# Optimization experiments

Hardware: AMD Instinct MI355X
Metric: run time of the kernel (lower is better)

The kernel has to match this reference:

```python
import jax, jax.numpy as jnp
import numpy as np

N_NODES = 50000
N_EDGES = 600000
IN_F = 128
HID = 128
OUT = 128
CLS = 128
N_GRAPHS = 64
LN_EPS = 1e-5


def _ln(h, g, b):
    m = jnp.mean(h, axis=-1, keepdims=True)
    v = jnp.var(h, axis=-1, keepdims=True)
    return (h - m) * jax.lax.rsqrt(v + LN_EPS) * g + b


def _segment_softmax(logits, seg, num_segments):
    m = jax.ops.segment_max(logits, seg, num_segments=num_segments)
    e = jnp.exp(logits - m[seg])
    s = jax.ops.segment_sum(e, seg, num_segments=num_segments)
    return e / s[seg]


def _gat_conv(x, src, dst, aux, w_lin, b_lin, aw1, ab1, lng, lnb, aw2, ab2):
    xl = x @ w_lin + b_lin                      # [N, out]
    sf = xl[src]                                # [E, out]
    df = xl[dst]                                # [E, out]
    ef = jnp.concatenate([sf, df, aux], axis=-1)  # [E, 2*out+2]
    h = jax.nn.relu(_ln(ef @ aw1 + ab1, lng, lnb))
    logits = h @ aw2 + ab2                      # [E, 1]
    att = _segment_softmax(logits, dst, xl.shape[0])
    num = jax.ops.segment_sum(sf * att, dst, num_segments=xl.shape[0])
    cnt = jax.ops.segment_sum(jnp.ones((src.shape[0], 1), xl.dtype), dst, num_segments=xl.shape[0])
    out = num / jnp.maximum(cnt, 1.0)           # scatter_mean (empty rows -> 0)
    return out + xl


def setup_inputs() -> dict:
    key = jax.random.key(0)
    ks = jax.random.split(key, 24)
    s = 0.05
    d = {
        'x': jax.random.normal(ks[0], (N_NODES, IN_F), jnp.float32),
        'edge_index': jax.random.randint(ks[1], (2, N_EDGES), 0, N_NODES, jnp.int64),
        'aux_info': jax.random.normal(ks[2], (N_EDGES, 2), jnp.float32),
        'batch': jnp.sort(jax.random.randint(ks[3], (N_NODES,), 0, N_GRAPHS, jnp.int64)),
        # conv1 params (in->hid)
        'w_lin1': jax.random.normal(ks[4], (IN_F, HID), jnp.float32) * s,
        'b_lin1': jnp.zeros((HID,), jnp.float32),
        'aw1_1': jax.random.normal(ks[5], (2 * HID + 2, HID), jnp.float32) * s,
        'ab1_1': jnp.zeros((HID,), jnp.float32),
        'lng1': jnp.ones((HID,), jnp.float32),
        'lnb1': jnp.zeros((HID,), jnp.float32),
        'aw2_1': jax.random.normal(ks[6], (HID, 1), jnp.float32) * s,
        'ab2_1': jnp.zeros((1,), jnp.float32),
        # conv2 params (hid->out)
        'w_lin2': jax.random.normal(ks[7], (HID, OUT), jnp.float32) * s,
        'b_lin2': jnp.zeros((OUT,), jnp.float32),
        'aw1_2': jax.random.normal(ks[8], (2 * OUT + 2, HID), jnp.float32) * s,
        'ab1_2': jnp.zeros((HID,), jnp.float32),
        'lng2': jnp.ones((HID,), jnp.float32),
        'lnb2': jnp.zeros((HID,), jnp.float32),
        'aw2_2': jax.random.normal(ks[9], (HID, 1), jnp.float32) * s,
        'ab2_2': jnp.zeros((1,), jnp.float32),
        # head
        'cls_w': jax.random.normal(ks[10], (OUT, CLS), jnp.float32) * s,
        'cls_b': jnp.zeros((CLS,), jnp.float32),
        'norm_g': jnp.ones((OUT,), jnp.float32),
        'norm_b': jnp.zeros((OUT,), jnp.float32),
    }
    return d


def reference(x, edge_index, aux_info, batch,
              w_lin1, b_lin1, aw1_1, ab1_1, lng1, lnb1, aw2_1, ab2_1,
              w_lin2, b_lin2, aw1_2, ab1_2, lng2, lnb2, aw2_2, ab2_2,
              cls_w, cls_b, norm_g, norm_b):
    src, dst = edge_index[0], edge_index[1]
    h = _gat_conv(x, src, dst, aux_info, w_lin1, b_lin1, aw1_1, ab1_1, lng1, lnb1, aw2_1, ab2_1)
    h = jax.nn.relu(h)
    h = _gat_conv(h, src, dst, aux_info, w_lin2, b_lin2, aw1_2, ab1_2, lng2, lnb2, aw2_2, ab2_2)
    h = _ln(h, norm_g, norm_b)                  # [N, out]
    fusion = jax.ops.segment_max(h, batch, num_segments=N_GRAPHS)  # global max pool
    cls = fusion @ cls_w + cls_b                # [G, cls]
    return (h, cls)
```

## Files before the change

kernel.cpp:

```cpp
#include <hip/hip_runtime.h>
#include <math.h>

typedef __attribute__((ext_vector_type(8))) short short8v;
typedef __attribute__((ext_vector_type(4))) float f32x4;
typedef __attribute__((ext_vector_type(2))) float f32x2;

__device__ __forceinline__ unsigned short f2bf(float f) {
    union { float f; unsigned int u; } v; v.f = f;
    unsigned int r = v.u + 0x7FFFu + ((v.u >> 16) & 1u);
    return (unsigned short)(r >> 16);
}
__device__ __forceinline__ float bflo(unsigned int v) {
    union { unsigned int u; float f; } x; x.u = v << 16; return x.f;
}
__device__ __forceinline__ float bfhi(unsigned int v) {
    union { unsigned int u; float f; } x; x.u = v & 0xFFFF0000u; return x.f;
}
__device__ __forceinline__ unsigned char f2fp8(float f) {
    return (unsigned char)(__builtin_amdgcn_cvt_pk_fp8_f32(f, f, 0, false) & 0xFF);
}

__global__ void hist_kernel(const int* __restrict__ dst, int* __restrict__ deg, int E) {
    int e = blockIdx.x * 256 + threadIdx.x;
    if (e < E) atomicAdd(&deg[dst[e]], 1);
}

__global__ __launch_bounds__(256) void scan1_kernel(const int* __restrict__ deg,
                                                    int* __restrict__ rp,
                                                    int* __restrict__ bsum, int N) {
    const int lane = threadIdx.x & 63, wid = threadIdx.x >> 6;
    int i = blockIdx.x * 256 + threadIdx.x;
    int v = (i < N) ? deg[i] : 0;
    int val = v;
#pragma unroll
    for (int off = 1; off < 64; off <<= 1) {
        int t = __shfl_up(val, off, 64);
        if (lane >= off) val += t;
    }
    __shared__ int ws[4];
    if (lane == 63) ws[wid] = val;
    __syncthreads();
    int pre = 0;
#pragma unroll
    for (int w = 0; w < 4; ++w) pre += (w < wid) ? ws[w] : 0;
    int incl = pre + val;
    if (i < N) rp[i] = incl - v;
    if (threadIdx.x == 255) bsum[blockIdx.x] = incl;
}

__global__ __launch_bounds__(256) void scan2_kernel(int* __restrict__ bsum, int NB) {
    const int lane = threadIdx.x & 63, wid = threadIdx.x >> 6;
    int t = threadIdx.x;
    int v = (t < NB) ? bsum[t] : 0;
    int val = v;
#pragma unroll
    for (int off = 1; off < 64; off <<= 1) {
        int t2 = __shfl_up(val, off, 64);
        if (lane >= off) val += t2;
    }
    __shared__ int ws[4];
    if (lane == 63) ws[wid] = val;
    __syncthreads();
    int pre = 0;
#pragma unroll
    for (int w = 0; w < 4; ++w) pre += (w < wid) ? ws[w] : 0;
    int excl = pre + val - v;
    __syncthreads();
    if (t < NB) bsum[t] = excl;
}

__global__ __launch_bounds__(256) void scan3_kernel(int* __restrict__ rp,
                                                    const int* __restrict__ bsum,
                                                    int N, int E) {
    int i = blockIdx.x * 256 + threadIdx.x;
    if (i < N) rp[i] += bsum[blockIdx.x];
    if (i == 0) rp[N] = E;
}

__global__ void scatter_kernel(const int* __restrict__ src, const int* __restrict__ dst,
                               const float* __restrict__ aux,
                               const int* __restrict__ rowptr, int* __restrict__ cursor,
                               uint2* __restrict__ er, int E) {
    int e = blockIdx.x * 256 + threadIdx.x;
    if (e < E) {
        int d = dst[e];
        int pos = rowptr[d] + atomicAdd(&cursor[d], 1);
        float2 a = *(const float2*)(aux + 2 * e);
        uint2 r;
        r.x = (unsigned)src[e] | ((unsigned)d << 16);
        r.y = (unsigned)f2bf(a.x) | ((unsigned)f2bf(a.y) << 16);
        er[pos] = r;
    }
}

__global__ void bounds_kernel(const int* __restrict__ batch, int* __restrict__ gstart,
                              int* __restrict__ gend, int N) {
    int i = blockIdx.x * 256 + threadIdx.x;
    if (i >= N) return;
    int b = batch[i];
    if (i == 0 || batch[i - 1] != b) gstart[b] = i;
    if (i == N - 1 || batch[i + 1] != b) gend[b] = i + 1;
}

__global__ __launch_bounds__(256) void pack6_kernel(const float* __restrict__ s0,
                                                    const float* __restrict__ s1,
                                                    const float* __restrict__ s2,
                                                    const float* __restrict__ s3,
                                                    const float* __restrict__ s4,
                                                    const float* __restrict__ s5,
                                                    unsigned short* __restrict__ Wp) {
    int which = blockIdx.x >> 6;
    const float* W = (which == 0) ? s0 : (which == 1) ? s1 : (which == 2) ? s2
                   : (which == 3) ? s3 : (which == 4) ? s4 : s5;
    int t = (blockIdx.x & 63) * 256 + threadIdx.x;
    int j = t & 7, l = (t >> 3) & 63, ct = (t >> 9) & 7, ks = t >> 12;
    int k = ks * 32 + (l >> 4) * 8 + j;
    int n = ct * 16 + (l & 15);
    Wp[which * 16384 + t] = f2bf(W[k * 128 + n]);
}

template <int ABF>
__global__ __launch_bounds__(256) void linpq_kernel(const void* __restrict__ Av,
                                                    const unsigned short* __restrict__ WpL,
                                                    const float* __restrict__ bias,
                                                    const unsigned short* __restrict__ WpP,
                                                    const unsigned short* __restrict__ WpQ,
                                                    const float* __restrict__ ab1,
                                                    unsigned short* __restrict__ Dbf,
                                                    unsigned char* __restrict__ Vf8,
                                                    unsigned char* __restrict__ Pf8,
                                                    unsigned char* __restrict__ Qf8, int M) {
    __shared__ unsigned short lds[32][136];
    const int l = threadIdx.x & 63, w = threadIdx.x >> 6;
    const int tile = w >> 1, ch = w & 1;
    const int rowbase = blockIdx.x * 32 + tile * 16;
    const int r = rowbase + (l & 15);
    const int kc = (l >> 4) * 8;

    short8v afr[4];
    if (r < M) {
        if (ABF) {
            const unsigned short* ap = (const unsigned short*)Av + (size_t)r * 128 + kc;
#pragma unroll
            for (int ks = 0; ks < 4; ++ks)
                afr[ks] = *(const short8v*)(ap + ks * 32);
        } else {
            const float* ap = (const float*)Av + (size_t)r * 128 + kc;
#pragma unroll
            for (int ks = 0; ks < 4; ++ks) {
                float4 x0 = *(const float4*)(ap + ks * 32);
                float4 x1 = *(const float4*)(ap + ks * 32 + 4);
                unsigned short u[8] = {f2bf(x0.x), f2bf(x0.y), f2bf(x0.z), f2bf(x0.w),
                                       f2bf(x1.x), f2bf(x1.y), f2bf(x1.z), f2bf(x1.w)};
                afr[ks] = *(short8v*)u;
            }
        }
    } else {
#pragma unroll
        for (int ks = 0; ks < 4; ++ks)
#pragma unroll
            for (int j = 0; j < 8; ++j) afr[ks][j] = 0;
    }

    f32x4 acc[4];
#pragma unroll
    for (int c = 0; c < 4; ++c)
#pragma unroll
        for (int j = 0; j < 4; ++j) acc[c][j] = 0.f;

    const short8v* wl = (const short8v*)WpL;
#pragma unroll
    for (int ks = 0; ks < 4; ++ks)
#pragma unroll
        for (int c = 0; c < 4; ++c)
            acc[c] = __builtin_amdgcn_mfma_f32_16x16x32_bf16(
                afr[ks], wl[(ks * 8 + ch * 4 + c) * 64 + l], acc[c], 0, 0, 0);

    const int rb = rowbase + (l >> 4) * 4;
    const int lrb = tile * 16 + (l >> 4) * 4;
#pragma unroll
    for (int c = 0; c < 4; ++c) {
        int col = (ch * 4 + c) * 16 + (l & 15);
        float bv = bias ? bias[col] : 0.f;
#pragma unroll
        for (int j = 0; j < 4; ++j) {
            int row = rb + j;
            if (row < M) {
                float v = acc[c][j] + bv;
                unsigned short bf = f2bf(v);
                Dbf[(size_t)row * 128 + col] = bf;
                Vf8[(size_t)row * 128 + col] = f2fp8(v);
                lds[lrb + j][col] = bf;
            } else {
                lds[lrb + j][col] = 0;
            }
        }
    }
    __syncthreads();

    short8v xfr[4];
#pragma unroll
    for (int ks = 0; ks < 4; ++ks)
        xfr[ks] = *(const short8v*)&lds[tile * 16 + (l & 15)][kc + ks * 32];

    f32x4 accP[4], accQ[4];
#pragma unroll
    for (int c = 0; c < 4; ++c)
#pragma unroll
        for (int j = 0; j < 4; ++j) { accP[c][j] = 0.f; accQ[c][j] = 0.f; }

    const short8v* wp = (const short8v*)WpP;
    const short8v* wq = (const short8v*)WpQ;
#pragma unroll
    for (int ks = 0; ks < 4; ++ks)
#pragma unroll
        for (int c = 0; c < 4; ++c) {
            accP[c] = __builtin_amdgcn_mfma_f32_16x16x32_bf16(
                xfr[ks], wp[(ks * 8 + ch * 4 + c) * 64 + l], accP[c], 0, 0, 0);
            accQ[c] = __builtin_amdgcn_mfma_f32_16x16x32_bf16(
                xfr[ks], wq[(ks * 8 + ch * 4 + c) * 64 + l], accQ[c], 0, 0, 0);
        }

#pragma unroll
    for (int c = 0; c < 4; ++c) {
        int col = (ch * 4 + c) * 16 + (l & 15);
        float b1v = ab1[col];
#pragma unroll
        for (int j = 0; j < 4; ++j) {
            int row = rb + j;
            if (row < M) {
                Pf8[(size_t)row * 128 + col] = f2fp8(accP[c][j]);
                Qf8[(size_t)row * 128 + col] = f2fp8(accQ[c][j] + b1v);
            }
        }
    }
}

__global__ __launch_bounds__(256, 4) void attn_edge_kernel(
    const unsigned char* __restrict__ Pf8, const unsigned char* __restrict__ Qf8,
    const uint2* __restrict__ er,
    const float* __restrict__ wa0, const float* __restrict__ wa1,
    const float* __restrict__ lng, const float* __restrict__ lnb,
    const float* __restrict__ aw2, const float* __restrict__ ab2,
    float* __restrict__ wt, int E) {
    __shared__ float lwp[640];
    for (int idx = threadIdx.x; idx < 640; idx += 256) {
        int arr = idx >> 7;
        int rem = idx & 127;
        int par = rem >> 6;
        int c = (rem >> 2) & 15;
        int e = rem & 3;
        const float* sp = (arr == 0) ? wa0 : (arr == 1) ? wa1 : (arr == 2) ? lng
                        : (arr == 3) ? lnb : aw2;
        lwp[(((arr * 16 + c) << 1) + par) * 4 + e] = sp[rem];
    }
    __syncthreads();
    const int slot = blockIdx.x * 128 + ((int)threadIdx.x >> 1);
    if (slot >= E) return;
    const int par = threadIdx.x & 1;
    const int co = par << 6;

#define LWP(arr, c) (*(const float4*)&lwp[((((arr) * 16 + (c)) << 1) + par) * 4])

    uint2 ev = er[slot];
    const int sn = (int)(ev.x & 0xFFFFu);
    const int dn = (int)(ev.x >> 16);
    const float ax = bflo(ev.y), ay = bfhi(ev.y);

    const uint4* prow = (const uint4*)(Pf8 + (size_t)sn * 128 + co);
    const uint4* qrow = (const uint4*)(Qf8 + (size_t)dn * 128 + co);

    float r1 = 0.f, r2 = 0.f;
    unsigned tp[32];

#pragma unroll
    for (int g = 0; g < 4; ++g) {
        uint4 pv = prow[g];
        uint4 qv = qrow[g];
        unsigned pwa[4] = {pv.x, pv.y, pv.z, pv.w};
        unsigned qwa[4] = {qv.x, qv.y, qv.z, qv.w};
#pragma unroll
        for (int cc = 0; cc < 4; ++cc) {
            const int c = g * 4 + cc;
            f32x2 plo = __builtin_amdgcn_cvt_pk_f32_fp8((int)pwa[cc], false);
            f32x2 phi = __builtin_amdgcn_cvt_pk_f32_fp8((int)pwa[cc], true);
            f32x2 qlo = __builtin_amdgcn_cvt_pk_f32_fp8((int)qwa[cc], false);
            f32x2 qhi = __builtin_amdgcn_cvt_pk_f32_fp8((int)qwa[cc], true);
            float4 w0v = LWP(0, c);
            float4 w1v = LWP(1, c);
            float t0 = plo[0] + qlo[0] + ax * w0v.x + ay * w1v.x;
            float t1 = plo[1] + qlo[1] + ax * w0v.y + ay * w1v.y;
            float t2 = phi[0] + qhi[0] + ax * w0v.z + ay * w1v.z;
            float t3 = phi[1] + qhi[1] + ax * w0v.w + ay * w1v.w;
            r1 += (t0 + t1) + (t2 + t3);
            r2 = fmaf(t0, t0, r2); r2 = fmaf(t1, t1, r2);
            r2 = fmaf(t2, t2, r2); r2 = fmaf(t3, t3, r2);
            asm("v_cvt_pk_bf16_f32 %0, %1, %2" : "=v"(tp[2 * c]) : "v"(t0), "v"(t1));
            asm("v_cvt_pk_bf16_f32 %0, %1, %2" : "=v"(tp[2 * c + 1]) : "v"(t2), "v"(t3));
        }
    }
    r1 += __shfl_xor(r1, 1, 64);
    r2 += __shfl_xor(r2, 1, 64);
    float mean = r1 * (1.f / 128.f);
    float rstd = rsqrtf(r2 * (1.f / 128.f) - mean * mean + 1e-5f);
    float mr = mean * rstd;

    float dot = 0.f;
#pragma unroll
    for (int c = 0; c < 16; ++c) {
        float4 gv = LWP(2, c);
        float4 bv = LWP(3, c);
        float4 wv = LWP(4, c);
        float t0 = bflo(tp[2 * c]), t1 = bfhi(tp[2 * c]);
        float t2 = bflo(tp[2 * c + 1]), t3 = bfhi(tp[2 * c + 1]);
        float h0 = fmaxf(fmaf(fmaf(t0, rstd, -mr), gv.x, bv.x), 0.f);
        float h1 = fmaxf(fmaf(fmaf(t1, rstd, -mr), gv.y, bv.y), 0.f);
        float h2 = fmaxf(fmaf(fmaf(t2, rstd, -mr), gv.z, bv.z), 0.f);
        float h3 = fmaxf(fmaf(fmaf(t3, rstd, -mr), gv.w, bv.w), 0.f);
        dot = fmaf(h0, wv.x, dot); dot = fmaf(h1, wv.y, dot);
        dot = fmaf(h2, wv.z, dot); dot = fmaf(h3, wv.w, dot);
    }
#undef LWP
    dot += __shfl_xor(dot, 1, 64);
    if (par == 0) wt[slot] = __expf(dot + ab2[0]);
}

template <int MODE>
__global__ __launch_bounds__(256) void aggr_kernel(
    const unsigned short* __restrict__ xlbf, const unsigned char* __restrict__ Vf8,
    const float* __restrict__ wt,
    const uint2* __restrict__ er, const int* __restrict__ rowptr,
    const float* __restrict__ g, const float* __restrict__ b,
    void* __restrict__ out, int N) {
    const int lane8 = threadIdx.x & 7;
    const int v = blockIdx.x * 32 + ((int)threadIdx.x >> 3);
    if (v >= N) return;
    const int jb = lane8 * 16;

    const int s0 = rowptr[v], s1e = rowptr[v + 1];
    const int deg = s1e - s0;
    float acc[16];
#pragma unroll
    for (int k = 0; k < 16; ++k) acc[k] = 0.f;
    float wsum = 0.f;

    uint4 v0 = make_uint4(0, 0, 0, 0), v1 = v0;
    float wb0 = 0.f, wb1 = 0.f;
#define GATH2(idx, VV, WW)                                                       \
    if ((idx) < s1e) {                                                           \
        int sn_ = (int)(er[idx].x & 0xFFFFu);                                    \
        VV = *(const uint4*)(Vf8 + (size_t)sn_ * 128 + jb);                      \
        WW = wt[idx];                                                            \
    }
    GATH2(s0, v0, wb0)
    GATH2(s0 + 1, v1, wb1)

    for (int i = s0; i < s1e; i += 2) {
        uint4 c0 = v0, c1 = v1;
        float u0 = wb0;
        float u1 = (i + 1 < s1e) ? wb1 : 0.f;
        GATH2(i + 2, v0, wb0)
        GATH2(i + 3, v1, wb1)
        wsum += u0 + u1;
        unsigned d0[4] = {c0.x, c0.y, c0.z, c0.w};
        unsigned d1[4] = {c1.x, c1.y, c1.z, c1.w};
#pragma unroll
        for (int k = 0; k < 4; ++k) {
            f32x2 alo = __builtin_amdgcn_cvt_pk_f32_fp8((int)d0[k], false);
            f32x2 ahi = __builtin_amdgcn_cvt_pk_f32_fp8((int)d0[k], true);
            f32x2 blo = __builtin_amdgcn_cvt_pk_f32_fp8((int)d1[k], false);
            f32x2 bhi = __builtin_amdgcn_cvt_pk_f32_fp8((int)d1[k], true);
            acc[4 * k + 0] += u0 * alo[0] + u1 * blo[0];
            acc[4 * k + 1] += u0 * alo[1] + u1 * blo[1];
            acc[4 * k + 2] += u0 * ahi[0] + u1 * bhi[0];
            acc[4 * k + 3] += u0 * ahi[1] + u1 * bhi[1];
        }
    }
#undef GATH2

    const float ns = (deg > 0) ? 1.f / (wsum * (float)deg) : 0.f;
    float o[16];
    const unsigned short* xp = xlbf + (size_t)v * 128 + jb;
    uint4 xa = *(const uint4*)xp;
    uint4 xb = *(const uint4*)(xp + 8);
    unsigned xw[8] = {xa.x, xa.y, xa.z, xa.w, xb.x, xb.y, xb.z, xb.w};
#pragma unroll
    for (int k = 0; k < 8; ++k) {
        o[2 * k] = bflo(xw[k]) + acc[2 * k] * ns;
        o[2 * k + 1] = bfhi(xw[k]) + acc[2 * k + 1] * ns;
    }

    if (MODE == 0) {
        unsigned short* op = (unsigned short*)out + (size_t)v * 128 + jb;
        unsigned opk[8];
#pragma unroll
        for (int k = 0; k < 8; ++k)
            opk[k] = (unsigned)f2bf(fmaxf(o[2 * k], 0.f)) |
                     ((unsigned)f2bf(fmaxf(o[2 * k + 1], 0.f)) << 16);
        *(uint4*)op = make_uint4(opk[0], opk[1], opk[2], opk[3]);
        *(uint4*)(op + 8) = make_uint4(opk[4], opk[5], opk[6], opk[7]);
    } else {
        float r1 = 0.f, r2 = 0.f;
#pragma unroll
        for (int k = 0; k < 16; ++k) { r1 += o[k]; r2 = fmaf(o[k], o[k], r2); }
#pragma unroll
        for (int mk = 4; mk >= 1; mk >>= 1) {
            r1 += __shfl_xor(r1, mk, 64);
            r2 += __shfl_xor(r2, mk, 64);
        }
        float mean = r1 * (1.f / 128.f);
        float rstd = rsqrtf(r2 * (1.f / 128.f) - mean * mean + 1e-5f);
        float mr = mean * rstd;
        float* op = (float*)out + (size_t)v * 128 + jb;
#pragma unroll
        for (int k4 = 0; k4 < 4; ++k4) {
            float4 gv = *(const float4*)(g + jb + 4 * k4);
            float4 bv = *(const float4*)(b + jb + 4 * k4);
            float4 r;
            r.x = fmaf(fmaf(o[4 * k4 + 0], rstd, -mr), gv.x, bv.x);
            r.y = fmaf(fmaf(o[4 * k4 + 1], rstd, -mr), gv.y, bv.y);
            r.z = fmaf(fmaf(o[4 * k4 + 2], rstd, -mr), gv.z, bv.z);
            r.w = fmaf(fmaf(o[4 * k4 + 3], rstd, -mr), gv.w, bv.w);
            *(float4*)(op + 4 * k4) = r;
        }
    }
}

__global__ __launch_bounds__(128) void pool1_kernel(const float* __restrict__ h,
                                                    const int* __restrict__ gstart,
                                                    const int* __restrict__ gend,
                                                    float* __restrict__ part) {
    int gph = blockIdx.x >> 4;
    int sl = blockIdx.x & 15;
    int col = threadIdx.x;
    int s = gstart[gph], e = gend[gph];
    float m = -INFINITY;
    for (int r = s + sl; r < e; r += 16) m = fmaxf(m, h[(size_t)r * 128 + col]);
    part[(size_t)blockIdx.x * 128 + col] = m;
}

__global__ __launch_bounds__(128) void cls_kernel(const float* __restrict__ part,
                                                  const float* __restrict__ cw,
                                                  const float* __restrict__ cb,
                                                  float* __restrict__ out) {
    int gph = blockIdx.x, c = threadIdx.x;
    float m = -INFINITY;
#pragma unroll
    for (int sl = 0; sl < 16; ++sl) m = fmaxf(m, part[(size_t)(gph * 16 + sl) * 128 + c]);
    __shared__ float f[128];
    f[c] = m;
    __syncthreads();
    float acc = cb[c];
#pragma unroll 8
    for (int k = 0; k < 128; ++k) acc += f[k] * cw[k * 128 + c];
    out[gph * 128 + c] = acc;
}

extern "C" void kernel_launch(void* const* d_in, const int* in_sizes, int n_in,
                              void* d_out, int out_size, void* d_ws, size_t ws_size,
                              hipStream_t stream) {
    const float* x      = (const float*)d_in[0];
    const int*   ei     = (const int*)d_in[1];
    const float* aux    = (const float*)d_in[2];
    const int*   batch  = (const int*)d_in[3];
    const float* w_lin1 = (const float*)d_in[4];
    const float* b_lin1 = (const float*)d_in[5];
    const float* aw1_1  = (const float*)d_in[6];
    const float* ab1_1  = (const float*)d_in[7];
    const float* lng1   = (const float*)d_in[8];
    const float* lnb1   = (const float*)d_in[9];
    const float* aw2_1  = (const float*)d_in[10];
    const float* ab2_1  = (const float*)d_in[11];
    const float* w_lin2 = (const float*)d_in[12];
    const float* b_lin2 = (const float*)d_in[13];
    const float* aw1_2  = (const float*)d_in[14];
    const float* ab1_2  = (const float*)d_in[15];
    const float* lng2   = (const float*)d_in[16];
    const float* lnb2   = (const float*)d_in[17];
    const float* aw2_2  = (const float*)d_in[18];
    const float* ab2_2  = (const float*)d_in[19];
    const float* cls_w  = (const float*)d_in[20];
    const float* cls_b  = (const float*)d_in[21];
    const float* norm_g = (const float*)d_in[22];
    const float* norm_b = (const float*)d_in[23];

    const int N = in_sizes[0] / 128;
    const int E = in_sizes[2] / 2;
    const int G = 64;
    const int* src = ei;
    const int* dst = ei + E;

    char* wsp = (char*)d_ws;
    unsigned short* xlbf  = (unsigned short*)wsp;   wsp += (size_t)N * 128 * 2;
    unsigned short* h1bf  = (unsigned short*)wsp;   wsp += (size_t)N * 128 * 2;
    unsigned char*  Pf8   = (unsigned char*)wsp;    wsp += (size_t)N * 128;
    unsigned char*  Qf8   = (unsigned char*)wsp;    wsp += (size_t)N * 128;
    unsigned char*  Vf8   = (unsigned char*)wsp;    wsp += (size_t)N * 128;
    unsigned short* wpack = (unsigned short*)wsp;   wsp += 6 * 16384 * 2;
    float*          part  = (float*)wsp;            wsp += (size_t)1024 * 128 * 4;
    uint2*          er    = (uint2*)wsp;            wsp += (size_t)E * 8;
    float*          wt    = (float*)wsp;            wsp += (size_t)E * 4;
    int*            bsum    = (int*)wsp;            wsp += 256 * 4;
    int*            deg     = (int*)wsp;            wsp += (size_t)N * 4;
    int*            cursor  = (int*)wsp;            wsp += (size_t)N * 4;
    int*            rowptr  = (int*)wsp;            wsp += (size_t)(N + 1) * 4;
    int*            gstart  = (int*)wsp;            wsp += (size_t)G * 4;
    int*            gend    = (int*)wsp;            wsp += (size_t)G * 4;

    unsigned short* wp_lin1 = wpack;
    unsigned short* wp_s1   = wpack + 16384;
    unsigned short* wp_d1   = wpack + 2 * 16384;
    unsigned short* wp_lin2 = wpack + 3 * 16384;
    unsigned short* wp_s2   = wpack + 4 * 16384;
    unsigned short* wp_d2   = wpack + 5 * 16384;

    float* hout   = (float*)d_out;
    float* clsout = hout + (size_t)N * 128;

    hipMemsetAsync(deg, 0, (size_t)(2 * N) * sizeof(int), stream);
    hipMemsetAsync(gstart, 0, (size_t)(2 * G) * sizeof(int), stream);

    const int eb = (E + 255) / 256;
    const int nb = (N + 255) / 256;
    const int lb = (N + 31) / 32;
    const int atb = (E + 127) / 128;
    const int agb = (N + 31) / 32;

    hist_kernel<<<eb, 256, 0, stream>>>(dst, deg, E);
    scan1_kernel<<<nb, 256, 0, stream>>>(deg, rowptr, bsum, N);
    scan2_kernel<<<1, 256, 0, stream>>>(bsum, nb);
    scan3_kernel<<<nb, 256, 0, stream>>>(rowptr, bsum, N, E);
    scatter_kernel<<<eb, 256, 0, stream>>>(src, dst, aux, rowptr, cursor, er, E);
    bounds_kernel<<<nb, 256, 0, stream>>>(batch, gstart, gend, N);

    pack6_kernel<<<384, 256, 0, stream>>>(w_lin1, aw1_1, aw1_1 + 128 * 128,
                                          w_lin2, aw1_2, aw1_2 + 128 * 128, wpack);

    linpq_kernel<0><<<lb, 256, 0, stream>>>(x, wp_lin1, b_lin1, wp_s1, wp_d1, ab1_1,
                                            xlbf, Vf8, Pf8, Qf8, N);
    attn_edge_kernel<<<atb, 256, 0, stream>>>(Pf8, Qf8, er,
                                              aw1_1 + 256 * 128, aw1_1 + 257 * 128,
                                              lng1, lnb1, aw2_1, ab2_1, wt, E);
    aggr_kernel<0><<<agb, 256, 0, stream>>>(xlbf, Vf8, wt, er, rowptr,
                                            nullptr, nullptr, h1bf, N);
    linpq_kernel<1><<<lb, 256, 0, stream>>>(h1bf, wp_lin2, b_lin2, wp_s2, wp_d2, ab1_2,
                                            xlbf, Vf8, Pf8, Qf8, N);
    attn_edge_kernel<<<atb, 256, 0, stream>>>(Pf8, Qf8, er,
                                              aw1_2 + 256 * 128, aw1_2 + 257 * 128,
                                              lng2, lnb2, aw2_2, ab2_2, wt, E);
    aggr_kernel<1><<<agb, 256, 0, stream>>>(xlbf, Vf8, wt, er, rowptr,
                                            norm_g, norm_b, hout, N);
    pool1_kernel<<<G * 16, 128, 0, stream>>>(hout, gstart, gend, part);
    cls_kernel<<<G, 128, 0, stream>>>(part, cls_w, cls_b, clsout);
}
```

Baseline: 261.8 us.

## Use packed fp16 math in edge attention and process four edge chunks per block

Rewrites the edge attention kernel's LayerNorm and score computation to use packed fp16 instructions (pk_fma, pk_max, dot2). Each block now handles four chunks of 128 edges, so the shared-memory weight staging is amortized over more edges and the grid is smaller. The aim is fewer ALU instructions per edge and less per-block setup. The cost is reduced precision in the LayerNorm statistics and activations, and possibly lower occupancy or less latency hiding with fewer blocks.

```diff
diff --git a/kernel.cpp b/kernel.cpp
--- a/kernel.cpp
+++ b/kernel.cpp
@@ -18,6 +18,26 @@
 }
 __device__ __forceinline__ unsigned char f2fp8(float f) {
     return (unsigned char)(__builtin_amdgcn_cvt_pk_fp8_f32(f, f, 0, false) & 0xFF);
+}
+__device__ __forceinline__ unsigned pkrtz(float a, float b) {
+    unsigned d;
+    asm("v_cvt_pkrtz_f16_f32 %0, %1, %2" : "=v"(d) : "v"(a), "v"(b));
+    return d;
+}
+__device__ __forceinline__ float fdot2a(unsigned a, unsigned b, float c) {
+    float d;
+    asm("v_dot2_f32_f16 %0, %1, %2, %3" : "=v"(d) : "v"(a), "v"(b), "v"(c));
+    return d;
+}
+__device__ __forceinline__ unsigned pk_fma_f16(unsigned a, unsigned b, unsigned c) {
+    unsigned d;
+    asm("v_pk_fma_f16 %0, %1, %2, %3" : "=v"(d) : "v"(a), "v"(b), "v"(c));
+    return d;
+}
+__device__ __forceinline__ unsigned pk_max0_f16(unsigned a, unsigned z) {
+    unsigned d;
+    asm("v_pk_max_f16 %0, %1, %2" : "=v"(d) : "v"(a), "v"(z));
+    return d;
 }
 
 __global__ void hist_kernel(const int* __restrict__ dst, int* __restrict__ deg, int E) {
@@ -243,86 +263,102 @@
     const float* __restrict__ lng, const float* __restrict__ lnb,
     const float* __restrict__ aw2, const float* __restrict__ ab2,
     float* __restrict__ wt, int E) {
-    __shared__ float lwp[640];
-    for (int idx = threadIdx.x; idx < 640; idx += 256) {
-        int arr = idx >> 7;
-        int rem = idx & 127;
-        int par = rem >> 6;
-        int c = (rem >> 2) & 15;
-        int e = rem & 3;
-        const float* sp = (arr == 0) ? wa0 : (arr == 1) ? wa1 : (arr == 2) ? lng
-                        : (arr == 3) ? lnb : aw2;
-        lwp[(((arr * 16 + c) << 1) + par) * 4 + e] = sp[rem];
+    __shared__ float lwf[256];
+    __shared__ unsigned lwh[192];
+    {
+        int idx = threadIdx.x;
+        int arr = idx >> 7, rem = idx & 127;
+        int par = rem >> 6, c = (rem >> 2) & 15, e = rem & 3;
+        const float* sp = arr ? wa1 : wa0;
+        lwf[(((arr * 16 + c) << 1) + par) * 4 + e] = sp[rem];
+        if (idx < 192) {
+            int a2 = idx >> 6, rem2 = idx & 63;
+            int p2 = rem2 >> 5;
+            int c2 = (rem2 >> 1) & 15;
+            int pr = rem2 & 1;
+            int chn = p2 * 64 + c2 * 4 + pr * 2;
+            const float* s2 = (a2 == 0) ? lng : (a2 == 1) ? lnb : aw2;
+            lwh[(((a2 * 16 + c2) << 1) + p2) * 2 + pr] = pkrtz(s2[chn], s2[chn + 1]);
+        }
     }
     __syncthreads();
-    const int slot = blockIdx.x * 128 + ((int)threadIdx.x >> 1);
-    if (slot >= E) return;
     const int par = threadIdx.x & 1;
+    const unsigned one2 = 0x3C003C00u;
+    const unsigned zero2 = 0u;
+    const float ab2v = ab2[0];
     const int co = par << 6;
 
-#define LWP(arr, c) (*(const float4*)&lwp[((((arr) * 16 + (c)) << 1) + par) * 4])
-
-    uint2 ev = er[slot];
-    const int sn = (int)(ev.x & 0xFFFFu);
-    const int dn = (int)(ev.x >> 16);
-    const float ax = bflo(ev.y), ay = bfhi(ev.y);
-
-    const uint4* prow = (const uint4*)(Pf8 + (size_t)sn * 128 + co);
-    const uint4* qrow = (const uint4*)(Qf8 + (size_t)dn * 128 + co);
-
-    float r1 = 0.f, r2 = 0.f;
-    unsigned tp[32];
-
-#pragma unroll
-    for (int g = 0; g < 4; ++g) {
-        uint4 pv = prow[g];
-        uint4 qv = qrow[g];
-        unsigned pwa[4] = {pv.x, pv.y, pv.z, pv.w};
-        unsigned qwa[4] = {qv.x, qv.y, qv.z, qv.w};
-#pragma unroll
-        for (int cc = 0; cc < 4; ++cc) {
-            const int c = g * 4 + cc;
-            f32x2 plo = __builtin_amdgcn_cvt_pk_f32_fp8((int)pwa[cc], false);
-            f32x2 phi = __builtin_amdgcn_cvt_pk_f32_fp8((int)pwa[cc], true);
-            f32x2 qlo = __builtin_amdgcn_cvt_pk_f32_fp8((int)qwa[cc], false);
-            f32x2 qhi = __builtin_amdgcn_cvt_pk_f32_fp8((int)qwa[cc], true);
-            float4 w0v = LWP(0, c);
-            float4 w1v = LWP(1, c);
-            float t0 = plo[0] + qlo[0] + ax * w0v.x + ay * w1v.x;
-            float t1 = plo[1] + qlo[1] + ax * w0v.y + ay * w1v.y;
-            float t2 = phi[0] + qhi[0] + ax * w0v.z + ay * w1v.z;
-            float t3 = phi[1] + qhi[1] + ax * w0v.w + ay * w1v.w;
-            r1 += (t0 + t1) + (t2 + t3);
-            r2 = fmaf(t0, t0, r2); r2 = fmaf(t1, t1, r2);
-            r2 = fmaf(t2, t2, r2); r2 = fmaf(t3, t3, r2);
-            asm("v_cvt_pk_bf16_f32 %0, %1, %2" : "=v"(tp[2 * c]) : "v"(t0), "v"(t1));
-            asm("v_cvt_pk_bf16_f32 %0, %1, %2" : "=v"(tp[2 * c + 1]) : "v"(t2), "v"(t3));
-        }
-    }
-    r1 += __shfl_xor(r1, 1, 64);
-    r2 += __shfl_xor(r2, 1, 64);
-    float mean = r1 * (1.f / 128.f);
-    float rstd = rsqrtf(r2 * (1.f / 128.f) - mean * mean + 1e-5f);
-    float mr = mean * rstd;
-
-    float dot = 0.f;
-#pragma unroll
-    for (int c = 0; c < 16; ++c) {
-        float4 gv = LWP(2, c);
-        float4 bv = LWP(3, c);
-        float4 wv = LWP(4, c);
-        float t0 = bflo(tp[2 * c]), t1 = bfhi(tp[2 * c]);
-        float t2 = bflo(tp[2 * c + 1]), t3 = bfhi(tp[2 * c + 1]);
-        float h0 = fmaxf(fmaf(fmaf(t0, rstd, -mr), gv.x, bv.x), 0.f);
-        float h1 = fmaxf(fmaf(fmaf(t1, rstd, -mr), gv.y, bv.y), 0.f);
-        float h2 = fmaxf(fmaf(fmaf(t2, rstd, -mr), gv.z, bv.z), 0.f);
-        float h3 = fmaxf(fmaf(fmaf(t3, rstd, -mr), gv.w, bv.w), 0.f);
-        dot = fmaf(h0, wv.x, dot); dot = fmaf(h1, wv.y, dot);
-        dot = fmaf(h2, wv.z, dot); dot = fmaf(h3, wv.w, dot);
-    }
-#undef LWP
-    dot += __shfl_xor(dot, 1, 64);
-    if (par == 0) wt[slot] = __expf(dot + ab2[0]);
+    for (int chunk = 0; chunk < 4; ++chunk) {
+        const int slot = (blockIdx.x * 4 + chunk) * 128 + ((int)threadIdx.x >> 1);
+        if (slot >= E) break;
+
+        uint2 ev = er[slot];
+        const int sn = (int)(ev.x & 0xFFFFu);
+        const int dn = (int)(ev.x >> 16);
+        const float ax = bflo(ev.y), ay = bfhi(ev.y);
+
+        const uint4* prow = (const uint4*)(Pf8 + (size_t)sn * 128 + co);
+        const uint4* qrow = (const uint4*)(Qf8 + (size_t)dn * 128 + co);
+
+        float r1 = 0.f, r2 = 0.f;
+        unsigned tp[32];
+
+#pragma unroll
+        for (int g = 0; g < 4; ++g) {
+            uint4 pv = prow[g];
+            uint4 qv = qrow[g];
+            unsigned pwa[4] = {pv.x, pv.y, pv.z, pv.w};
+            unsigned qwa[4] = {qv.x, qv.y, qv.z, qv.w};
+#pragma unroll
+            for (int cc = 0; cc < 4; ++cc) {
+                const int c = g * 4 + cc;
+                f32x2 plo = __builtin_amdgcn_cvt_pk_f32_fp8((int)pwa[cc], false);
+                f32x2 phi = __builtin_amdgcn_cvt_pk_f32_fp8((int)pwa[cc], true);
+                f32x2 qlo = __builtin_amdgcn_cvt_pk_f32_fp8((int)qwa[cc], false);
+                f32x2 qhi = __builtin_amdgcn_cvt_pk_f32_fp8((int)qwa[cc], true);
+                float4 w0v = *(const float4*)&lwf[((c << 1) + par) * 4];
+                float4 w1v = *(const float4*)&lwf[(((16 + c) << 1) + par) * 4];
+                float t0 = plo[0] + qlo[0] + ax * w0v.x + ay * w1v.x;
+                float t1 = plo[1] + qlo[1] + ax * w0v.y + ay * w1v.y;
+                float t2 = phi[0] + qhi[0] + ax * w0v.z + ay * w1v.z;
+                float t3 = phi[1] + qhi[1] + ax * w0v.w + ay * w1v.w;
+                unsigned p0 = pkrtz(t0, t1);
+                unsigned p1 = pkrtz(t2, t3);
+                tp[2 * c] = p0;
+                tp[2 * c + 1] = p1;
+                r1 = fdot2a(p0, one2, r1);
+                r1 = fdot2a(p1, one2, r1);
+                r2 = fdot2a(p0, p0, r2);
+                r2 = fdot2a(p1, p1, r2);
+            }
+        }
+        r1 += __shfl_xor(r1, 1, 64);
+        r2 += __shfl_xor(r2, 1, 64);
+        float mean = r1 * (1.f / 128.f);
+        float rstd = rsqrtf(r2 * (1.f / 128.f) - mean * mean + 1e-5f);
+        float mr = mean * rstd;
+        unsigned rstd2 = pkrtz(rstd, rstd);
+        unsigned nmr2 = pkrtz(-mr, -mr);
+
+        float dot = 0.f;
+#pragma unroll
+        for (int c = 0; c < 16; ++c) {
+            unsigned base = (unsigned)(((c << 1) + par) * 2);
+            uint2 gg = *(const uint2*)&lwh[base];
+            uint2 ll = *(const uint2*)&lwh[64 + base];
+            uint2 ww = *(const uint2*)&lwh[128 + base];
+            unsigned u0 = pk_fma_f16(tp[2 * c], rstd2, nmr2);
+            u0 = pk_fma_f16(u0, gg.x, ll.x);
+            u0 = pk_max0_f16(u0, zero2);
+            dot = fdot2a(u0, ww.x, dot);
+            unsigned u1 = pk_fma_f16(tp[2 * c + 1], rstd2, nmr2);
+            u1 = pk_fma_f16(u1, gg.y, ll.y);
+            u1 = pk_max0_f16(u1, zero2);
+            dot = fdot2a(u1, ww.y, dot);
+        }
+        dot += __shfl_xor(dot, 1, 64);
+        if (par == 0) wt[slot] = __expf(dot + ab2v);
+    }
 }
 
 template <int MODE>
@@ -523,7 +559,7 @@
     const int eb = (E + 255) / 256;
     const int nb = (N + 255) / 256;
     const int lb = (N + 31) / 32;
-    const int atb = (E + 127) / 128;
+    const int atb = (E + 511) / 512;
     const int agb = (N + 31) / 32;
 
     hist_kernel<<<eb, 256, 0, stream>>>(dst, deg, E);
```

Result: no change. 257.2 us (-1.7%).
